# Kernel optimization log

Hardware: AMD Instinct MI355X
Metric: run time of the kernel (lower is better)

## Reference

```python
import jax, jax.numpy as jnp
import numpy as np

N_NODES = 40000
N_EDGES = 640000
IN_C = 128
HID = 32
HEADS = 4
OUT_C = 8
NUM_GRAPHS = 64
NEG_SLOPE = 0.2


def setup_inputs() -> dict:
    key = jax.random.key(0)
    ks = jax.random.split(key, 16)
    x = jax.random.normal(ks[0], (N_NODES, IN_C), dtype=jnp.float32)
    edge_index = jax.random.randint(ks[1], (2, N_EDGES), 0, N_NODES, dtype=jnp.int64)
    batch = jnp.sort(jax.random.randint(ks[2], (N_NODES,), 0, NUM_GRAPHS, dtype=jnp.int64))
    s = lambda k, shape, fan_in: jax.random.normal(k, shape, jnp.float32) / np.sqrt(fan_in)
    # conv0: in -> hid, 4 heads, concat
    W0 = s(ks[3], (IN_C, HEADS * HID), IN_C)
    a_src0 = s(ks[4], (HEADS, HID), HID)
    a_dst0 = s(ks[5], (HEADS, HID), HID)
    b0 = jnp.zeros((HEADS * HID,), jnp.float32)
    # conv1: hid*H -> hid, 4 heads, concat
    W1 = s(ks[6], (HEADS * HID, HEADS * HID), HEADS * HID)
    a_src1 = s(ks[7], (HEADS, HID), HID)
    a_dst1 = s(ks[8], (HEADS, HID), HID)
    b1 = jnp.zeros((HEADS * HID,), jnp.float32)
    # conv2: hid*H -> hid, 1 head, no concat
    W2 = s(ks[9], (HEADS * HID, HID), HEADS * HID)
    a_src2 = s(ks[10], (1, HID), HID)
    a_dst2 = s(ks[11], (1, HID), HID)
    b2 = jnp.zeros((HID,), jnp.float32)
    lin1_w = s(ks[12], (HID, IN_C), HID)
    lin1_b = jnp.zeros((IN_C,), jnp.float32)
    lin2_w = s(ks[13], (IN_C, OUT_C), IN_C)
    lin2_b = jnp.zeros((OUT_C,), jnp.float32)
    return dict(x=x, edge_index=edge_index, batch=batch,
                W0=W0, a_src0=a_src0, a_dst0=a_dst0, b0=b0,
                W1=W1, a_src1=a_src1, a_dst1=a_dst1, b1=b1,
                W2=W2, a_src2=a_src2, a_dst2=a_dst2, b2=b2,
                lin1_w=lin1_w, lin1_b=lin1_b, lin2_w=lin2_w, lin2_b=lin2_b)


def gat_conv(x, src, dst, W, a_src, a_dst, b, heads, out_c, concat):
    N = x.shape[0]
    h = (x @ W).reshape(N, heads, out_c)          # [N,H,C]
    als = (h * a_src[None]).sum(-1)               # [N,H]
    ald = (h * a_dst[None]).sum(-1)               # [N,H]
    e = jax.nn.leaky_relu(als[src] + ald[dst], NEG_SLOPE)  # [E,H]
    m = jax.ops.segment_max(e, dst, num_segments=N)
    m = jnp.where(jnp.isfinite(m), m, 0.0)
    p = jnp.exp(e - m[dst])                       # [E,H]
    denom = jax.ops.segment_sum(p, dst, num_segments=N)
    alpha = p / jnp.maximum(denom[dst], 1e-16)
    out = jax.ops.segment_sum(h[src] * alpha[:, :, None], dst, num_segments=N)
    out = out.reshape(N, heads * out_c) if concat else out.mean(axis=1)
    return out + b


def reference(x, edge_index, batch,
              W0, a_src0, a_dst0, b0,
              W1, a_src1, a_dst1, b1,
              W2, a_src2, a_dst2, b2,
              lin1_w, lin1_b, lin2_w, lin2_b):
    N = x.shape[0]
    # PyG GATConv adds self-loops by default
    loop = jnp.arange(N, dtype=edge_index.dtype)
    src = jnp.concatenate([edge_index[0], loop])
    dst = jnp.concatenate([edge_index[1], loop])
    # eval mode: dropout is identity
    h = jax.nn.elu(gat_conv(x, src, dst, W0, a_src0, a_dst0, b0, HEADS, HID, True))
    h = jax.nn.elu(gat_conv(h, src, dst, W1, a_src1, a_dst1, b1, HEADS, HID, True))
    h = jax.nn.elu(gat_conv(h, src, dst, W2, a_src2, a_dst2, b2, 1, HID, False))
    # global mean pool over graphs
    sums = jax.ops.segment_sum(h, batch, num_segments=NUM_GRAPHS)
    cnts = jax.ops.segment_sum(jnp.ones((N, 1), h.dtype), batch, num_segments=NUM_GRAPHS)
    g = sums / jnp.maximum(cnts, 1.0)             # [G, HID]
    g = jax.nn.relu(g @ lin1_w + lin1_b)
    return g @ lin2_w + lin2_b                    # [G, OUT_C]
```

## Files before the change

### kernel.cpp

```cpp
#include <hip/hip_runtime.h>
#include <hip/hip_bf16.h>

#define N_NODES 40000
#define N_EDGES 640000
#define E_TOT   (N_EDGES + N_NODES)
#define NUM_GRAPHS 64
#define SCAN_BLOCKS 160
#define SCAN_CHUNK  250

typedef __attribute__((ext_vector_type(8))) short bf16x8;
typedef __attribute__((ext_vector_type(4))) float f32x4;

__device__ inline float bf2f(unsigned short u) {
    union { unsigned int i; float f; } v; v.i = ((unsigned int)u) << 16; return v.f;
}
__device__ inline unsigned short f2bf(float f) {
    union { float f; unsigned int i; } v; v.f = f;
    unsigned int r = v.i + 0x7FFF + ((v.i >> 16) & 1);
    return (unsigned short)(r >> 16);
}


__global__ __launch_bounds__(256) void cvt_x(const float* __restrict__ x,
                                             unsigned short* __restrict__ xb) {
    int i = blockIdx.x * 256 + threadIdx.x;
    float4 v = ((const float4*)x)[i];
    ushort4 o;
    o.x = f2bf(v.x); o.y = f2bf(v.y); o.z = f2bf(v.z); o.w = f2bf(v.w);
    ((ushort4*)xb)[i] = o;
}

__global__ __launch_bounds__(256) void cvt_w(const float* __restrict__ W0,
                                             const float* __restrict__ W1,
                                             const float* __restrict__ W2,
                                             unsigned short* __restrict__ Wt0,
                                             unsigned short* __restrict__ Wt1,
                                             unsigned short* __restrict__ Wt2) {
    int idx = blockIdx.x * 256 + threadIdx.x;
    if (idx < 16384) {
        int n = idx >> 7, k = idx & 127;
        Wt0[idx] = f2bf(W0[k * 128 + n]);
    } else if (idx < 32768) {
        int i = idx - 16384;
        int n = i >> 7, k = i & 127;
        Wt1[i] = f2bf(W1[k * 128 + n]);
    } else if (idx < 36864) {
        int i = idx - 32768;
        int n = i >> 7, k = i & 127;
        Wt2[i] = f2bf(W2[k * 32 + n]);
    }
}


__global__ __launch_bounds__(256) void hist_rank_kernel(const int* __restrict__ edst,
                                                        int* __restrict__ counts,
                                                        int* __restrict__ rank) {
    int e = blockIdx.x * 256 + threadIdx.x;
    if (e >= E_TOT) return;
    int d = (e < N_EDGES) ? edst[e] : (e - N_EDGES);
    rank[e] = atomicAdd(&counts[d], 1);
}

__global__ __launch_bounds__(256) void bsum_kernel(const int* __restrict__ counts,
                                                   int* __restrict__ bsum) {
    __shared__ int ws[4];
    int b = blockIdx.x, tid = threadIdx.x;
    int idx = b * SCAN_CHUNK + tid;
    int v = (tid < SCAN_CHUNK) ? counts[idx] : 0;
#pragma unroll
    for (int off = 32; off >= 1; off >>= 1) v += __shfl_down(v, off, 64);
    if ((tid & 63) == 0) ws[tid >> 6] = v;
    __syncthreads();
    if (tid == 0) bsum[b] = ws[0] + ws[1] + ws[2] + ws[3];
}

__global__ __launch_bounds__(256) void bscan_kernel(const int* __restrict__ bsum,
                                                    int* __restrict__ bofs) {
    __shared__ int s[256];
    int tid = threadIdx.x;
    int v = (tid < SCAN_BLOCKS) ? bsum[tid] : 0;
    s[tid] = v;
    __syncthreads();
    for (int off = 1; off < 256; off <<= 1) {
        int t = (tid >= off) ? s[tid - off] : 0;
        __syncthreads();
        s[tid] += t;
        __syncthreads();
    }
    if (tid < SCAN_BLOCKS) bofs[tid] = s[tid] - v;
}

__global__ __launch_bounds__(256) void boffs_kernel(const int* __restrict__ counts,
                                                    const int* __restrict__ bofs,
                                                    int* __restrict__ offs) {
    __shared__ int s[256];
    int b = blockIdx.x, tid = threadIdx.x;
    int idx = b * SCAN_CHUNK + tid;
    int v = (tid < SCAN_CHUNK) ? counts[idx] : 0;
    s[tid] = v;
    __syncthreads();
    for (int off = 1; off < 256; off <<= 1) {
        int t = (tid >= off) ? s[tid - off] : 0;
        __syncthreads();
        s[tid] += t;
        __syncthreads();
    }
    int incl = s[tid];
    int base = bofs[b];
    if (tid < SCAN_CHUNK) {
        offs[idx] = base + incl - v;
        if (idx == N_NODES - 1) offs[N_NODES] = base + incl;
    }
}

__global__ __launch_bounds__(256) void scatter_kernel(const int* __restrict__ esrc,
                                                      const int* __restrict__ edst,
                                                      const int* __restrict__ offs,
                                                      const int* __restrict__ rank,
                                                      int* __restrict__ ssrc) {
    int e = blockIdx.x * 256 + threadIdx.x;
    if (e >= E_TOT) return;
    int d, s;
    if (e < N_EDGES) { d = edst[e]; s = esrc[e]; }
    else             { d = e - N_EDGES; s = d; }
    ssrc[offs[d] + rank[e]] = s;
}

__global__ __launch_bounds__(256) void gemm128_mfma(const unsigned short* __restrict__ Xb,
                                                    const unsigned short* __restrict__ Wt,
                                                    const float* __restrict__ asrc,
                                                    const float* __restrict__ adst,
                                                    unsigned short* __restrict__ Hb,
                                                    float* __restrict__ ALS,
                                                    float* __restrict__ ALD) {
    int wave = threadIdx.x >> 6;
    int lane = threadIdx.x & 63;
    int l15 = lane & 15;
    int q = lane >> 4;
    int r0 = (blockIdx.x * 4 + wave) * 16;

    f32x4 acc[8];
#pragma unroll
    for (int t = 0; t < 8; ++t) acc[t] = (f32x4){0.f, 0.f, 0.f, 0.f};

    float asv[8], adv[8];
#pragma unroll
    for (int t = 0; t < 8; ++t) {
        int c = t * 16 + l15;
        asv[t] = asrc[c];
        adv[t] = adst[c];
    }

    const unsigned short* xrow = Xb + (long)(r0 + l15) * 128 + q * 8;
    const unsigned short* wrow = Wt + (long)l15 * 128 + q * 8;
#pragma unroll
    for (int kt = 0; kt < 4; ++kt) {
        bf16x8 a = *(const bf16x8*)(xrow + kt * 32);
#pragma unroll
        for (int t = 0; t < 8; ++t) {
            bf16x8 b = *(const bf16x8*)(wrow + (long)t * 16 * 128 + kt * 32);
            acc[t] = __builtin_amdgcn_mfma_f32_16x16x32_bf16(a, b, acc[t], 0, 0, 0);
        }
    }

#pragma unroll
    for (int t = 0; t < 8; ++t)
#pragma unroll
        for (int i = 0; i < 4; ++i)
            Hb[(long)(r0 + q * 4 + i) * 128 + t * 16 + l15] = f2bf(acc[t][i]);

#pragma unroll
    for (int i = 0; i < 4; ++i) {
        float ps0 = acc[0][i] * asv[0] + acc[1][i] * asv[1];
        float ps1 = acc[2][i] * asv[2] + acc[3][i] * asv[3];
        float ps2 = acc[4][i] * asv[4] + acc[5][i] * asv[5];
        float ps3 = acc[6][i] * asv[6] + acc[7][i] * asv[7];
        float pd0 = acc[0][i] * adv[0] + acc[1][i] * adv[1];
        float pd1 = acc[2][i] * adv[2] + acc[3][i] * adv[3];
        float pd2 = acc[4][i] * adv[4] + acc[5][i] * adv[5];
        float pd3 = acc[6][i] * adv[6] + acc[7][i] * adv[7];
#pragma unroll
        for (int m = 1; m < 16; m <<= 1) {
            ps0 += __shfl_xor(ps0, m, 16); ps1 += __shfl_xor(ps1, m, 16);
            ps2 += __shfl_xor(ps2, m, 16); ps3 += __shfl_xor(ps3, m, 16);
            pd0 += __shfl_xor(pd0, m, 16); pd1 += __shfl_xor(pd1, m, 16);
            pd2 += __shfl_xor(pd2, m, 16); pd3 += __shfl_xor(pd3, m, 16);
        }
        if (l15 == 0) {
            int r = r0 + q * 4 + i;
            *(float4*)(ALS + (long)r * 4) = make_float4(ps0, ps1, ps2, ps3);
            *(float4*)(ALD + (long)r * 4) = make_float4(pd0, pd1, pd2, pd3);
        }
    }
}

__global__ __launch_bounds__(256) void gemm32_mfma(const unsigned short* __restrict__ Xb,
                                                   const unsigned short* __restrict__ Wt2,
                                                   const float* __restrict__ asrc,
                                                   const float* __restrict__ adst,
                                                   unsigned short* __restrict__ H2b,
                                                   float* __restrict__ ALS,
                                                   float* __restrict__ ALD) {
    int wave = threadIdx.x >> 6;
    int lane = threadIdx.x & 63;
    int l15 = lane & 15;
    int q = lane >> 4;
    int r0 = (blockIdx.x * 4 + wave) * 16;

    f32x4 acc[2];
    acc[0] = (f32x4){0.f, 0.f, 0.f, 0.f};
    acc[1] = (f32x4){0.f, 0.f, 0.f, 0.f};

    const unsigned short* xrow = Xb + (long)(r0 + l15) * 128 + q * 8;
    const unsigned short* wrow = Wt2 + (long)l15 * 128 + q * 8;
#pragma unroll
    for (int kt = 0; kt < 4; ++kt) {
        bf16x8 a = *(const bf16x8*)(xrow + kt * 32);
#pragma unroll
        for (int t = 0; t < 2; ++t) {
            bf16x8 b = *(const bf16x8*)(wrow + (long)t * 16 * 128 + kt * 32);
            acc[t] = __builtin_amdgcn_mfma_f32_16x16x32_bf16(a, b, acc[t], 0, 0, 0);
        }
    }

    float as0 = asrc[l15], as1 = asrc[16 + l15];
    float ad0 = adst[l15], ad1 = adst[16 + l15];
#pragma unroll
    for (int t = 0; t < 2; ++t)
#pragma unroll
        for (int i = 0; i < 4; ++i)
            H2b[(long)(r0 + q * 4 + i) * 32 + t * 16 + l15] = f2bf(acc[t][i]);

#pragma unroll
    for (int i = 0; i < 4; ++i) {
        float ps = acc[0][i] * as0 + acc[1][i] * as1;
        float pd = acc[0][i] * ad0 + acc[1][i] * ad1;
#pragma unroll
        for (int m = 1; m < 16; m <<= 1) {
            ps += __shfl_xor(ps, m, 16);
            pd += __shfl_xor(pd, m, 16);
        }
        if (l15 == 0) {
            int r = r0 + q * 4 + i;
            ALS[r] = ps;
            ALD[r] = pd;
        }
    }
}

__global__ __launch_bounds__(256) void agg128(const unsigned short* __restrict__ Hb,
                                              const float* __restrict__ ALS,
                                              const float* __restrict__ ALD,
                                              const int* __restrict__ offs,
                                              const int* __restrict__ ssrc,
                                              const float* __restrict__ bias,
                                              unsigned short* __restrict__ OUTb) {
    int n = blockIdx.x * 4 + (threadIdx.x >> 6);
    n = __builtin_amdgcn_readfirstlane(n);
    if (n >= N_NODES) return;
    int lane = threadIdx.x & 63;
    int c = lane * 2;
    int head = lane >> 4;
    int e16 = lane & 15;
    float aldh = ALD[n * 4 + head];
    int j0 = __builtin_amdgcn_readfirstlane(offs[n]);
    int j1 = __builtin_amdgcn_readfirstlane(offs[n + 1]);
    float a0 = 0.f, a1 = 0.f, dsum = 0.f;
    for (int jb = j0; jb < j1; jb += 16) {
        int j = jb + e16;
        int jc = (j < j1) ? j : (j1 - 1);
        int s = ssrc[jc];
        float4 als4 = *(const float4*)(ALS + (long)s * 4);
        float alsv = (head == 0) ? als4.x : (head == 1) ? als4.y
                   : (head == 2) ? als4.z : als4.w;
        float e = alsv + aldh;
        e = (e > 0.f) ? e : 0.2f * e;
        float w = (j < j1) ? __expf(e) : 0.f;
        int st[16]; float wt[16];
#pragma unroll
        for (int t = 0; t < 16; ++t) {
            st[t] = __shfl(s, t, 16);
            wt[t] = __shfl(w, t, 16);
        }
        unsigned int hv[16];
#pragma unroll
        for (int t = 0; t < 16; ++t)
            hv[t] = *(const unsigned int*)(Hb + (long)st[t] * 128 + c);
#pragma unroll
        for (int t = 0; t < 16; ++t) {
            float h0 = bf2f((unsigned short)(hv[t] & 0xFFFF));
            float h1 = bf2f((unsigned short)(hv[t] >> 16));
            dsum += wt[t];
            a0 += wt[t] * h0;
            a1 += wt[t] * h1;
        }
    }
    float inv = 1.0f / dsum;
    float o0 = a0 * inv + bias[c];
    float o1 = a1 * inv + bias[c + 1];
    o0 = (o0 > 0.f) ? o0 : (__expf(o0) - 1.f);
    o1 = (o1 > 0.f) ? o1 : (__expf(o1) - 1.f);
    ushort2 ob; ob.x = f2bf(o0); ob.y = f2bf(o1);
    *(ushort2*)(OUTb + (long)n * 128 + c) = ob;
}

__global__ __launch_bounds__(256) void agg32(const unsigned short* __restrict__ H2b,
                                             const float* __restrict__ ALS,
                                             const float* __restrict__ ALD,
                                             const int* __restrict__ offs,
                                             const int* __restrict__ ssrc,
                                             const float* __restrict__ bias,
                                             float* __restrict__ OUT) {
    int wv = blockIdx.x * 4 + (threadIdx.x >> 6);
    int lane = threadIdx.x & 63;
    int col = lane & 31;
    int half = lane >> 5;
    int e16 = lane & 15;
    int n = wv * 2 + half;
    if (n >= N_NODES) return;
    float aldn = ALD[n];
    int j0 = offs[n], j1 = offs[n + 1];
    float a = 0.f, dsum = 0.f;
    for (int jb = j0; jb < j1; jb += 16) {
        int j = jb + e16;
        int jc = (j < j1) ? j : (j1 - 1);
        int s = ssrc[jc];
        float e = ALS[s] + aldn;
        e = (e > 0.f) ? e : 0.2f * e;
        float w = (j < j1) ? __expf(e) : 0.f;
        int st[16]; float wt[16];
#pragma unroll
        for (int t = 0; t < 16; ++t) {
            st[t] = __shfl(s, t, 16);
            wt[t] = __shfl(w, t, 16);
        }
        unsigned short hv[16];
#pragma unroll
        for (int t = 0; t < 16; ++t)
            hv[t] = H2b[st[t] * 32 + col];
#pragma unroll
        for (int t = 0; t < 16; ++t) {
            dsum += wt[t];
            a += wt[t] * bf2f(hv[t]);
        }
    }
    float o = a / dsum + bias[col];
    o = (o > 0.f) ? o : (__expf(o) - 1.f);
    OUT[n * 32 + col] = o;
}

__global__ __launch_bounds__(256) void pool_kernel(const float* __restrict__ H3,
                                                   const int* __restrict__ batch,
                                                   float* __restrict__ gsum,
                                                   float* __restrict__ gcnt) {
    const int CHUNK = 40;
    int gid = (blockIdx.x * 256 + threadIdx.x) >> 5;
    int c = threadIdx.x & 31;
    int n0 = gid * CHUNK;
    if (n0 >= N_NODES) return;
    int n1 = n0 + CHUNK;
    if (n1 > N_NODES) n1 = N_NODES;
    int cur = batch[n0];
    float acc = 0.f;
    int cnt = 0;
    for (int n = n0; n < n1; ++n) {
        int b = batch[n];
        if (b != cur) {
            atomicAdd(&gsum[cur * 32 + c], acc);
            if (c == 0) atomicAdd(&gcnt[cur], (float)cnt);
            cur = b; acc = 0.f; cnt = 0;
        }
        acc += H3[n * 32 + c];
        cnt++;
    }
    atomicAdd(&gsum[cur * 32 + c], acc);
    if (c == 0) atomicAdd(&gcnt[cur], (float)cnt);
}

__global__ __launch_bounds__(256) void mlp_kernel(const float* __restrict__ gsum,
                                                  const float* __restrict__ gcnt,
                                                  const float* __restrict__ l1w,
                                                  const float* __restrict__ l1b,
                                                  const float* __restrict__ l2w,
                                                  const float* __restrict__ l2b,
                                                  float* __restrict__ out) {
    __shared__ float g[NUM_GRAPHS * 32];
    __shared__ float t1[NUM_GRAPHS * 128];
    int tid = threadIdx.x;
    for (int i = tid; i < NUM_GRAPHS * 32; i += 256) {
        float c = gcnt[i >> 5];
        g[i] = gsum[i] / fmaxf(c, 1.0f);
    }
    __syncthreads();
    for (int i = tid; i < NUM_GRAPHS * 128; i += 256) {
        int r = i >> 7, j = i & 127;
        float a = l1b[j];
        for (int k = 0; k < 32; ++k) a += g[r * 32 + k] * l1w[k * 128 + j];
        t1[i] = fmaxf(a, 0.f);
    }
    __syncthreads();
    for (int i = tid; i < NUM_GRAPHS * 8; i += 256) {
        int r = i >> 3, j = i & 7;
        float a = l2b[j];
        for (int k = 0; k < 128; ++k) a += t1[r * 128 + k] * l2w[k * 8 + j];
        out[i] = a;
    }
}


extern "C" void kernel_launch(void* const* d_in, const int* in_sizes, int n_in,
                              void* d_out, int out_size, void* d_ws, size_t ws_size,
                              hipStream_t stream) {
    const float* x      = (const float*)d_in[0];
    const int*   eidx   = (const int*)d_in[1];
    const int*   batch  = (const int*)d_in[2];
    const float* W0     = (const float*)d_in[3];
    const float* asrc0  = (const float*)d_in[4];
    const float* adst0  = (const float*)d_in[5];
    const float* b0     = (const float*)d_in[6];
    const float* W1     = (const float*)d_in[7];
    const float* asrc1  = (const float*)d_in[8];
    const float* adst1  = (const float*)d_in[9];
    const float* b1     = (const float*)d_in[10];
    const float* W2     = (const float*)d_in[11];
    const float* asrc2  = (const float*)d_in[12];
    const float* adst2  = (const float*)d_in[13];
    const float* b2     = (const float*)d_in[14];
    const float* l1w    = (const float*)d_in[15];
    const float* l1b    = (const float*)d_in[16];
    const float* l2w    = (const float*)d_in[17];
    const float* l2b    = (const float*)d_in[18];
    float* out = (float*)d_out;

    const int* esrc = eidx;
    const int* edst = eidx + N_EDGES;

    float* ALS  = (float*)d_ws;
    float* ALD  = ALS + N_NODES * 4;
    float* h3   = ALD + N_NODES * 4;
    int* counts = (int*)(h3 + (long)N_NODES * 32);
    float* gsum = (float*)(counts + N_NODES);
    float* gcnt = gsum + NUM_GRAPHS * 32;
    int* offs   = (int*)(gcnt + NUM_GRAPHS);
    int* bsum   = offs + (N_NODES + 1);
    int* bofs   = bsum + SCAN_BLOCKS;
    int* rank   = bofs + SCAN_BLOCKS;
    int* ssrc   = rank + E_TOT;
    uintptr_t p = (uintptr_t)(ssrc + E_TOT);
    p = (p + 15) & ~(uintptr_t)15;
    unsigned short* Xb   = (unsigned short*)p;
    unsigned short* Hb   = Xb + (long)N_NODES * 128;
    unsigned short* OUTb = Hb + (long)N_NODES * 128;
    unsigned short* H2b  = OUTb + (long)N_NODES * 128;
    unsigned short* Wt0  = H2b + (long)N_NODES * 32;
    unsigned short* Wt1  = Wt0 + 128 * 128;
    unsigned short* Wt2  = Wt1 + 128 * 128;

    size_t zbytes = (size_t)(N_NODES + NUM_GRAPHS * 32 + NUM_GRAPHS) * 4;
    hipMemsetAsync(counts, 0, zbytes, stream);

    cvt_x<<<5000, 256, 0, stream>>>(x, Xb);
    cvt_w<<<144, 256, 0, stream>>>(W0, W1, W2, Wt0, Wt1, Wt2);

    int eblocks = (E_TOT + 255) / 256;
    hist_rank_kernel<<<eblocks, 256, 0, stream>>>(edst, counts, rank);
    bsum_kernel<<<SCAN_BLOCKS, 256, 0, stream>>>(counts, bsum);
    bscan_kernel<<<1, 256, 0, stream>>>(bsum, bofs);
    boffs_kernel<<<SCAN_BLOCKS, 256, 0, stream>>>(counts, bofs, offs);
    scatter_kernel<<<eblocks, 256, 0, stream>>>(esrc, edst, offs, rank, ssrc);

    gemm128_mfma<<<625, 256, 0, stream>>>(Xb, Wt0, asrc0, adst0, Hb, ALS, ALD);
    agg128<<<10000, 256, 0, stream>>>(Hb, ALS, ALD, offs, ssrc, b0, OUTb);

    gemm128_mfma<<<625, 256, 0, stream>>>(OUTb, Wt1, asrc1, adst1, Hb, ALS, ALD);
    agg128<<<10000, 256, 0, stream>>>(Hb, ALS, ALD, offs, ssrc, b1, OUTb);

    gemm32_mfma<<<625, 256, 0, stream>>>(OUTb, Wt2, asrc2, adst2, H2b, ALS, ALD);
    agg32<<<5000, 256, 0, stream>>>(H2b, ALS, ALD, offs, ssrc, b2, h3);

    pool_kernel<<<125, 256, 0, stream>>>(h3, batch, gsum, gcnt);
    mlp_kernel<<<1, 256, 0, stream>>>(gsum, gcnt, l1w, l1b, l2w, l2b, out);
}
```

Measured before the change: 314.1 us.

## Fuse setup kernels with zeroing and store attention logits head-major

Merges the x conversion, weight conversion and the memset into a single launch so two launches and a memset call go away. It also changes the per-node attention logits ALS/ALD from node-major [N,4] to head-major [4,N] layout. In agg128 each lane then gathers one scalar for its own head instead of a float4 followed by a select. The layout change cuts gather bytes per edge in the aggregation, at the cost of scattered scalar stores in the GEMM epilogue.

```diff
diff --git a/kernel.cpp b/kernel.cpp
--- a/kernel.cpp
+++ b/kernel.cpp
@@ -8,6 +8,11 @@
 #define SCAN_BLOCKS 160
 #define SCAN_CHUNK  250
 
+#define CVTX_BLOCKS 5000
+#define CVTW_BLOCKS 144
+#define ZERO_INTS   (N_NODES + NUM_GRAPHS * 32 + NUM_GRAPHS)
+#define ZERO_BLOCKS ((ZERO_INTS + 255) / 256)
+
 typedef __attribute__((ext_vector_type(8))) short bf16x8;
 typedef __attribute__((ext_vector_type(4))) float f32x4;
 
@@ -21,33 +26,40 @@
 }
 
 
-__global__ __launch_bounds__(256) void cvt_x(const float* __restrict__ x,
-                                             unsigned short* __restrict__ xb) {
-    int i = blockIdx.x * 256 + threadIdx.x;
-    float4 v = ((const float4*)x)[i];
-    ushort4 o;
-    o.x = f2bf(v.x); o.y = f2bf(v.y); o.z = f2bf(v.z); o.w = f2bf(v.w);
-    ((ushort4*)xb)[i] = o;
-}
-
-__global__ __launch_bounds__(256) void cvt_w(const float* __restrict__ W0,
-                                             const float* __restrict__ W1,
-                                             const float* __restrict__ W2,
-                                             unsigned short* __restrict__ Wt0,
-                                             unsigned short* __restrict__ Wt1,
-                                             unsigned short* __restrict__ Wt2) {
-    int idx = blockIdx.x * 256 + threadIdx.x;
-    if (idx < 16384) {
-        int n = idx >> 7, k = idx & 127;
-        Wt0[idx] = f2bf(W0[k * 128 + n]);
-    } else if (idx < 32768) {
-        int i = idx - 16384;
-        int n = i >> 7, k = i & 127;
-        Wt1[i] = f2bf(W1[k * 128 + n]);
-    } else if (idx < 36864) {
-        int i = idx - 32768;
-        int n = i >> 7, k = i & 127;
-        Wt2[i] = f2bf(W2[k * 32 + n]);
+__global__ __launch_bounds__(256) void setup_kernel(const float* __restrict__ x,
+                                                    const float* __restrict__ W0,
+                                                    const float* __restrict__ W1,
+                                                    const float* __restrict__ W2,
+                                                    unsigned short* __restrict__ Xb,
+                                                    unsigned short* __restrict__ Wt0,
+                                                    unsigned short* __restrict__ Wt1,
+                                                    unsigned short* __restrict__ Wt2,
+                                                    int* __restrict__ zbase) {
+    int b = blockIdx.x;
+    int tid = threadIdx.x;
+    if (b < CVTX_BLOCKS) {
+        int i = b * 256 + tid;
+        float4 v = ((const float4*)x)[i];
+        ushort4 o;
+        o.x = f2bf(v.x); o.y = f2bf(v.y); o.z = f2bf(v.z); o.w = f2bf(v.w);
+        ((ushort4*)Xb)[i] = o;
+    } else if (b < CVTX_BLOCKS + CVTW_BLOCKS) {
+        int idx = (b - CVTX_BLOCKS) * 256 + tid;
+        if (idx < 16384) {
+            int n = idx >> 7, k = idx & 127;
+            Wt0[idx] = f2bf(W0[k * 128 + n]);
+        } else if (idx < 32768) {
+            int i = idx - 16384;
+            int n = i >> 7, k = i & 127;
+            Wt1[i] = f2bf(W1[k * 128 + n]);
+        } else {
+            int i = idx - 32768;
+            int n = i >> 7, k = i & 127;
+            Wt2[i] = f2bf(W2[k * 32 + n]);
+        }
+    } else {
+        int i = (b - CVTX_BLOCKS - CVTW_BLOCKS) * 256 + tid;
+        if (i < ZERO_INTS) zbase[i] = 0;
     }
 }
 
@@ -131,8 +143,8 @@
                                                     const float* __restrict__ asrc,
                                                     const float* __restrict__ adst,
                                                     unsigned short* __restrict__ Hb,
-                                                    float* __restrict__ ALS,
-                                                    float* __restrict__ ALD) {
+                                                    float* __restrict__ ALS_t,
+                                                    float* __restrict__ ALD_t) {
     int wave = threadIdx.x >> 6;
     int lane = threadIdx.x & 63;
     int l15 = lane & 15;
@@ -186,10 +198,14 @@
             pd0 += __shfl_xor(pd0, m, 16); pd1 += __shfl_xor(pd1, m, 16);
             pd2 += __shfl_xor(pd2, m, 16); pd3 += __shfl_xor(pd3, m, 16);
         }
-        if (l15 == 0) {
-            int r = r0 + q * 4 + i;
-            *(float4*)(ALS + (long)r * 4) = make_float4(ps0, ps1, ps2, ps3);
-            *(float4*)(ALD + (long)r * 4) = make_float4(pd0, pd1, pd2, pd3);
+        int r = r0 + q * 4 + i;
+        if (l15 < 4) {
+            float v = (l15 == 0) ? ps0 : (l15 == 1) ? ps1 : (l15 == 2) ? ps2 : ps3;
+            ALS_t[l15 * N_NODES + r] = v;
+        } else if (l15 < 8) {
+            int h = l15 - 4;
+            float v = (h == 0) ? pd0 : (h == 1) ? pd1 : (h == 2) ? pd2 : pd3;
+            ALD_t[h * N_NODES + r] = v;
         }
     }
 }
@@ -249,8 +265,8 @@
 }
 
 __global__ __launch_bounds__(256) void agg128(const unsigned short* __restrict__ Hb,
-                                              const float* __restrict__ ALS,
-                                              const float* __restrict__ ALD,
+                                              const float* __restrict__ ALS_t,
+                                              const float* __restrict__ ALD_t,
                                               const int* __restrict__ offs,
                                               const int* __restrict__ ssrc,
                                               const float* __restrict__ bias,
@@ -262,7 +278,8 @@
     int c = lane * 2;
     int head = lane >> 4;
     int e16 = lane & 15;
-    float aldh = ALD[n * 4 + head];
+    float aldh = ALD_t[head * N_NODES + n];
+    const float* alsh = ALS_t + (long)head * N_NODES;
     int j0 = __builtin_amdgcn_readfirstlane(offs[n]);
     int j1 = __builtin_amdgcn_readfirstlane(offs[n + 1]);
     float a0 = 0.f, a1 = 0.f, dsum = 0.f;
@@ -270,10 +287,7 @@
         int j = jb + e16;
         int jc = (j < j1) ? j : (j1 - 1);
         int s = ssrc[jc];
-        float4 als4 = *(const float4*)(ALS + (long)s * 4);
-        float alsv = (head == 0) ? als4.x : (head == 1) ? als4.y
-                   : (head == 2) ? als4.z : als4.w;
-        float e = alsv + aldh;
+        float e = alsh[s] + aldh;
         e = (e > 0.f) ? e : 0.2f * e;
         float w = (j < j1) ? __expf(e) : 0.f;
         int st[16]; float wt[16];
@@ -456,11 +470,8 @@
     unsigned short* Wt1  = Wt0 + 128 * 128;
     unsigned short* Wt2  = Wt1 + 128 * 128;
 
-    size_t zbytes = (size_t)(N_NODES + NUM_GRAPHS * 32 + NUM_GRAPHS) * 4;
-    hipMemsetAsync(counts, 0, zbytes, stream);
-
-    cvt_x<<<5000, 256, 0, stream>>>(x, Xb);
-    cvt_w<<<144, 256, 0, stream>>>(W0, W1, W2, Wt0, Wt1, Wt2);
+    setup_kernel<<<CVTX_BLOCKS + CVTW_BLOCKS + ZERO_BLOCKS, 256, 0, stream>>>(
+        x, W0, W1, W2, Xb, Wt0, Wt1, Wt2, counts);
 
     int eblocks = (E_TOT + 255) / 256;
     hist_rank_kernel<<<eblocks, 256, 0, stream>>>(edst, counts, rank);
```

Result: no change. 313.5 us (-0.2%).
